# Performance work log

Hardware: AMD Instinct MI355X
Metric: run time of the kernel (lower is better)

Reference implementation:

```python
import jax, jax.numpy as jnp
import numpy as np

B, H, S, D = 2, 16, 2048, 64

def setup_inputs() -> dict:
    key = jax.random.key(0)
    kq, kk, kv, km = jax.random.split(key, 4)
    q = jax.random.normal(kq, (B, H, S, D), dtype=jnp.float32)
    k = jax.random.normal(kk, (B, H, S, D), dtype=jnp.float32)
    v = jax.random.normal(kv, (B, H, S, D), dtype=jnp.float32)
    mask = jax.random.randint(km, (B, 1, S, S), 0, 2, dtype=jnp.int32)
    return {"q": q, "k": k, "v": v, "mask": mask}

def reference(q, k, v, mask):
    d_k = q.shape[-1]
    # scores: [B, H, S, S]
    scores = jnp.einsum('bhqd,bhkd->bhqk', q, k) / jnp.sqrt(jnp.float32(d_k))
    scores = jnp.where(mask == 0, -jnp.inf, scores)
    attn = jax.nn.softmax(scores, axis=-1)
    return jnp.einsum('bhqk,bhkd->bhqd', attn, v)
```

## Files before the change

### kernel.cpp

```cpp
#include <hip/hip_runtime.h>
#include <hip/hip_bf16.h>

typedef unsigned short u16;
typedef unsigned int   u32;
typedef unsigned long long u64;
typedef __attribute__((ext_vector_type(8)))  __bf16 bf16x8;
typedef __attribute__((ext_vector_type(4)))  float  f32x4;
typedef __attribute__((ext_vector_type(16))) float  f32x16;
typedef __attribute__((ext_vector_type(8)))  u16    ushort8;
typedef __attribute__((ext_vector_type(4)))  u32    u32x4;

#define S_LEN 2048
#define D_DIM 64
#define NBH   32
#define SD    131072
#define MROW  32
#define MB_PB 65536
#define NT    32

#define KB_OFF 0u
#define VT_OFF 8388608u
#define MB_OFF 16777216u
#define WS_NEED 17825792u

#define QSCALE 0.18033688011112042f

static __device__ __forceinline__ u16 f2bf(float f) {
  u32 u = __builtin_bit_cast(u32, f);
  u += 0x7fffu + ((u >> 16) & 1u);
  return (u16)(u >> 16);
}

static __device__ __forceinline__ void gl16(const void* g, void* l) {
  __builtin_amdgcn_global_load_lds(
      (const __attribute__((address_space(1))) u32*)g,
      (__attribute__((address_space(3))) u32*)l, 16, 0, 0);
}

static __device__ __forceinline__ u32 cvtpk(float lo, float hi) {
  u32 d;
  asm("v_cvt_pk_bf16_f32 %0, %1, %2" : "=v"(d) : "v"(lo), "v"(hi));
  return d;
}
static __device__ __forceinline__ void plswap(u32& a, u32& b) {
  asm volatile("v_permlane32_swap_b32 %0, %1" : "+v"(a), "+v"(b));
}

#define WAITV(N) asm volatile("s_waitcnt vmcnt(" #N ")" ::: "memory")

__global__ __launch_bounds__(256) void prep_all(
    const float* __restrict__ K, const float* __restrict__ V, const int* __restrict__ M,
    u16* __restrict__ Kb, u16* __restrict__ Vt, u64* __restrict__ Mb) {
  const int bx = blockIdx.x, tid = threadIdx.x;
  if (bx < 2048) {
    size_t i = ((size_t)bx * 256 + tid) * 8;
    float4 a = *reinterpret_cast<const float4*>(K + i);
    float4 b = *reinterpret_cast<const float4*>(K + i + 4);
    ushort8 u;
    u[0]=f2bf(a.x); u[1]=f2bf(a.y); u[2]=f2bf(a.z); u[3]=f2bf(a.w);
    u[4]=f2bf(b.x); u[5]=f2bf(b.y); u[6]=f2bf(b.z); u[7]=f2bf(b.w);
    *reinterpret_cast<ushort8*>(Kb + i) = u;
  } else if (bx < 3072) {
    __shared__ u16 t[64][72];
    const int idx = bx - 2048;
    const int bh = idx >> 5, s0 = (idx & 31) * 64;
    const float* src = V + ((size_t)bh * S_LEN + s0) * D_DIM;
    const int r = tid >> 2, c0 = (tid & 3) * 16;
#pragma unroll
    for (int i = 0; i < 16; i += 4) {
      float4 x = *reinterpret_cast<const float4*>(src + r * 64 + c0 + i);
      t[r][c0+i]   = f2bf(x.x); t[r][c0+i+1] = f2bf(x.y);
      t[r][c0+i+2] = f2bf(x.z); t[r][c0+i+3] = f2bf(x.w);
    }
    __syncthreads();
    u16* dst = Vt + (size_t)bh * SD + s0;
#pragma unroll
    for (int qq = 0; qq < 2; ++qq) {
      int q = tid * 2 + qq;
      int d = q >> 3, so = (q & 7) * 8;
      ushort8 u;
#pragma unroll
      for (int j = 0; j < 8; ++j) u[j] = t[so + j][d];
      *reinterpret_cast<ushort8*>(dst + d * S_LEN + so) = u;
    }
  } else {
    int g = (bx - 3072) * 256 + tid;
    int lane = g & 63;
    int v = M[(size_t)g];
    u64 bits = __ballot(v != 0);
    if (lane == 0) Mb[g >> 6] = bits;
  }
}

static __device__ __forceinline__ void iter_body(
    const u16* kb, const u16* vb, u64 mw,
    const bf16x8* Qf, f32x16& accOT0, f32x16& accOT1, float& l_,
    int l31, int hi, int swz) {
  const u32 mlo = (u32)mw, mhiw = (u32)(mw >> 32);

  f32x16 sT0 = {0,0,0,0,0,0,0,0,0,0,0,0,0,0,0,0};
  f32x16 sT1 = {0,0,0,0,0,0,0,0,0,0,0,0,0,0,0,0};
  __builtin_amdgcn_s_setprio(1);
#pragma unroll
  for (int s = 0; s < 4; ++s) {
    bf16x8 k0 = *reinterpret_cast<const bf16x8*>(kb + l31 * 64        + ((s*2+hi) ^ swz) * 8);
    bf16x8 k1 = *reinterpret_cast<const bf16x8*>(kb + (32 + l31) * 64 + ((s*2+hi) ^ swz) * 8);
    sT0 = __builtin_amdgcn_mfma_f32_32x32x16_bf16(k0, Qf[s], sT0, 0, 0, 0);
    sT1 = __builtin_amdgcn_mfma_f32_32x32x16_bf16(k1, Qf[s], sT1, 0, 0, 0);
  }
  __builtin_amdgcn_s_setprio(0);

  float lp0 = 0.f, lp1 = 0.f, lp2 = 0.f, lp3 = 0.f;
  u32 A0_[8], A1_[8];
#pragma unroll
  for (int T = 0; T < 2; ++T) {
    const f32x16& sv = T ? sT1 : sT0;
    const u32 mword = T ? mhiw : mlo;
    float pr[16];
#pragma unroll
    for (int r = 0; r < 16; ++r) {
      const int bit = (r & 3) + 8 * (r >> 2) + 4 * hi;
      float e = __builtin_amdgcn_exp2f(sv[r]);
      int sx = __builtin_amdgcn_sbfe(mword, bit, 1);
      e = __builtin_bit_cast(float, __builtin_bit_cast(u32, e) & (u32)sx);
      if ((r & 3) == 0) lp0 += e; else if ((r & 3) == 1) lp1 += e;
      else if ((r & 3) == 2) lp2 += e; else lp3 += e;
      pr[r] = e;
    }
#pragma unroll
    for (int j = 0; j < 8; ++j) {
      u32 w = cvtpk(pr[2 * j], pr[2 * j + 1]);
      if (T == 0) A0_[j] = w; else A1_[j] = w;
    }
  }
  l_ += (lp0 + lp1) + (lp2 + lp3);

  bf16x8 PA[4];
  {
    u32 a, c, b2, d2;
    a = A0_[0]; c = A0_[2]; plswap(a, c);
    b2 = A0_[1]; d2 = A0_[3]; plswap(b2, d2);
    u32x4 w0 = {a, b2, c, d2}; PA[0] = __builtin_bit_cast(bf16x8, w0);
    a = A0_[4]; c = A0_[6]; plswap(a, c);
    b2 = A0_[5]; d2 = A0_[7]; plswap(b2, d2);
    u32x4 w1 = {a, b2, c, d2}; PA[1] = __builtin_bit_cast(bf16x8, w1);
    a = A1_[0]; c = A1_[2]; plswap(a, c);
    b2 = A1_[1]; d2 = A1_[3]; plswap(b2, d2);
    u32x4 w2 = {a, b2, c, d2}; PA[2] = __builtin_bit_cast(bf16x8, w2);
    a = A1_[4]; c = A1_[6]; plswap(a, c);
    b2 = A1_[5]; d2 = A1_[7]; plswap(b2, d2);
    u32x4 w3 = {a, b2, c, d2}; PA[3] = __builtin_bit_cast(bf16x8, w3);
  }

  __builtin_amdgcn_s_setprio(1);
#pragma unroll
  for (int ks = 0; ks < 4; ++ks) {
    bf16x8 v0 = *reinterpret_cast<const bf16x8*>(vb + l31 * 64        + ((ks*2+hi) ^ swz) * 8);
    bf16x8 v1 = *reinterpret_cast<const bf16x8*>(vb + (32 + l31) * 64 + ((ks*2+hi) ^ swz) * 8);
    accOT0 = __builtin_amdgcn_mfma_f32_32x32x16_bf16(v0, PA[ks], accOT0, 0, 0, 0);
    accOT1 = __builtin_amdgcn_mfma_f32_32x32x16_bf16(v1, PA[ks], accOT1, 0, 0, 0);
  }
  __builtin_amdgcn_s_setprio(0);
}

__global__ __launch_bounds__(256, 2) void attn_fwd5(
    const float* __restrict__ Q, const u16* __restrict__ Kb,
    const u16* __restrict__ Vt, const u64* __restrict__ Mb,
    float* __restrict__ O) {
  __shared__ __align__(16) u16 LB[32768];

  const int tid  = threadIdx.x;
  const int lane = tid & 63;
  const int wid  = tid >> 6;
  const int l31  = lane & 31;
  const int hi   = lane >> 5;
  const int swz  = l31 & 7;

  const int bh = blockIdx.y, b = bh >> 4;
  const int q0w = blockIdx.x * 128 + wid * 32;
  const size_t base = (size_t)bh * SD;

  bf16x8 Qf[4];
  {
    const float* qsrc = Q + base + (size_t)(q0w + l31) * 64;
#pragma unroll
    for (int s = 0; s < 4; ++s) {
      const int d0 = s * 16 + hi * 8;
      float4 x = *reinterpret_cast<const float4*>(qsrc + d0);
      float4 y = *reinterpret_cast<const float4*>(qsrc + d0 + 4);
      u32x4 w;
      w[0] = cvtpk(x.x * QSCALE, x.y * QSCALE);
      w[1] = cvtpk(x.z * QSCALE, x.w * QSCALE);
      w[2] = cvtpk(y.x * QSCALE, y.y * QSCALE);
      w[3] = cvtpk(y.z * QSCALE, y.w * QSCALE);
      Qf[s] = __builtin_bit_cast(bf16x8, w);
    }
  }

  const int srow = tid >> 3;
  const int sjx  = (tid & 7) ^ (srow & 7);
  const u16* ksA = Kb + base + srow * 64 + sjx * 8;
  const u16* vsA = Vt + base + (size_t)srow * S_LEN + sjx * 8;

  const u64* mp = Mb + (size_t)b * MB_PB + (size_t)(q0w + l31) * MROW;

  f32x16 accOT0 = {0,0,0,0,0,0,0,0,0,0,0,0,0,0,0,0};
  f32x16 accOT1 = {0,0,0,0,0,0,0,0,0,0,0,0,0,0,0,0};
  float l_ = 0.f;

#define STAGE(buf, it) do {                                                        \
    gl16(ksA + (size_t)(it) * 4096,        LB + (buf) * 4096 + tid * 8);           \
    gl16(ksA + (size_t)(it) * 4096 + 2048, LB + (buf) * 4096 + 2048 + tid * 8);    \
    gl16(vsA + (size_t)(it) * 64,          LB + 16384 + (buf) * 4096 + tid * 8);   \
    gl16(vsA + (size_t)(it) * 64 + 65536,  LB + 16384 + (buf) * 4096 + 2048 + tid * 8); \
  } while (0)

#define BODY(IT, J, WN, DOSTAGE) do {                                    \
    WAITV(WN);                                                            \
    __builtin_amdgcn_s_barrier();                                         \
    __builtin_amdgcn_sched_barrier(0);                                    \
    if (DOSTAGE) { STAGE((((J) + 3) & 3), (IT) + 3); }                    \
    iter_body(LB + (J) * 4096, LB + 16384 + (J) * 4096, cm[J],            \
              Qf, accOT0, accOT1, l_, l31, hi, swz);                      \
  } while (0)

  u64 cm[4], nm[4];
  cm[0] = mp[0]; cm[1] = mp[1]; cm[2] = mp[2]; cm[3] = mp[3];
  STAGE(0, 0); STAGE(1, 1); STAGE(2, 2);

#pragma unroll 1
  for (int g = 0; g < 7; ++g) {
    const int it0 = g * 4;
    nm[0] = mp[it0 + 4]; nm[1] = mp[it0 + 5];
    nm[2] = mp[it0 + 6]; nm[3] = mp[it0 + 7];
    BODY(it0 + 0, 0, 8, true);
    BODY(it0 + 1, 1, 8, true);
    BODY(it0 + 2, 2, 8, true);
    BODY(it0 + 3, 3, 8, true);
    cm[0] = nm[0]; cm[1] = nm[1]; cm[2] = nm[2]; cm[3] = nm[3];
  }
  BODY(28, 0, 8, true);
  BODY(29, 1, 8, false);
  BODY(30, 2, 4, false);
  BODY(31, 3, 0, false);

  __syncthreads();

  l_ += __shfl_xor(l_, 32);
  const float inv = __builtin_amdgcn_rcpf(l_);

  float* Sc = (float*)((char*)LB + wid * 4608);
#pragma unroll
  for (int D0 = 0; D0 < 2; ++D0) {
    const f32x16& acc = D0 ? accOT1 : accOT0;
#pragma unroll
    for (int r = 0; r < 16; ++r) {
      const int dloc = (r & 3) + 8 * (r >> 2) + 4 * hi;
      Sc[l31 * 36 + dloc] = acc[r] * inv;
    }
    asm volatile("s_waitcnt lgkmcnt(0)" ::: "memory");
    __builtin_amdgcn_sched_barrier(0);
    const int qq = lane >> 1, off = (lane & 1) * 16;
#pragma unroll
    for (int j = 0; j < 4; ++j) {
      float4 x = *reinterpret_cast<const float4*>(&Sc[qq * 36 + off + j * 4]);
      *reinterpret_cast<float4*>(O + base + (size_t)(q0w + qq) * 64 + D0 * 32 + off + j * 4) = x;
    }
    asm volatile("s_waitcnt lgkmcnt(0)" ::: "memory");
    __builtin_amdgcn_sched_barrier(0);
  }
#undef STAGE
#undef BODY
}

#define KST 72
#define VST 40
#define PST 40
static __device__ __forceinline__ bf16x8 ld_frag(const u16* p) {
  ushort8 u = *reinterpret_cast<const ushort8*>(p);
  return __builtin_bit_cast(bf16x8, u);
}
__global__ __launch_bounds__(256) void attn_fwd_v1(
    const float* __restrict__ Q, const float* __restrict__ K,
    const float* __restrict__ V, const int* __restrict__ M,
    float* __restrict__ O) {
  __shared__ __align__(16) u16 Klds[32 * KST];
  __shared__ __align__(16) u16 Vlds[64 * VST];
  __shared__ __align__(16) u16 Plds[4 * 16 * PST];
  const int tid = threadIdx.x, lane = tid & 63, wid = tid >> 6;
  const int lrow = lane & 15, lgrp = lane >> 4;
  const int bh = blockIdx.y, b = bh >> 4;
  const int q0 = blockIdx.x * 64 + wid * 16;
  const int base = bh * S_LEN * D_DIM, mbase = b * S_LEN * S_LEN;
  bf16x8 qf[2];
#pragma unroll
  for (int c = 0; c < 2; ++c) {
    const float* src = Q + base + (q0 + lrow) * 64 + c * 32 + lgrp * 8;
    float4 x = *reinterpret_cast<const float4*>(src);
    float4 y = *reinterpret_cast<const float4*>(src + 4);
    ushort8 u;
    u[0]=f2bf(x.x*0.125f); u[1]=f2bf(x.y*0.125f); u[2]=f2bf(x.z*0.125f); u[3]=f2bf(x.w*0.125f);
    u[4]=f2bf(y.x*0.125f); u[5]=f2bf(y.y*0.125f); u[6]=f2bf(y.z*0.125f); u[7]=f2bf(y.w*0.125f);
    qf[c] = __builtin_bit_cast(bf16x8, u);
  }
  f32x4 accO[4];
#pragma unroll
  for (int c = 0; c < 4; ++c) accO[c] = (f32x4){0.f,0.f,0.f,0.f};
  float m_[4] = {-1e9f,-1e9f,-1e9f,-1e9f}, l_[4] = {0.f,0.f,0.f,0.f};
  const int srow = tid >> 3, scol = (tid & 7) * 8;
  for (int kv0 = 0; kv0 < S_LEN; kv0 += 32) {
    __syncthreads();
    {
      const float* src = K + base + (kv0 + srow) * 64 + scol;
      float4 x = *reinterpret_cast<const float4*>(src);
      float4 y = *reinterpret_cast<const float4*>(src + 4);
      ushort8 u;
      u[0]=f2bf(x.x); u[1]=f2bf(x.y); u[2]=f2bf(x.z); u[3]=f2bf(x.w);
      u[4]=f2bf(y.x); u[5]=f2bf(y.y); u[6]=f2bf(y.z); u[7]=f2bf(y.w);
      *reinterpret_cast<ushort8*>(&Klds[srow * KST + scol]) = u;
    }
    {
      const float* src = V + base + (kv0 + srow) * 64 + scol;
      float4 x = *reinterpret_cast<const float4*>(src);
      float4 y = *reinterpret_cast<const float4*>(src + 4);
      float vals[8] = {x.x,x.y,x.z,x.w,y.x,y.y,y.z,y.w};
#pragma unroll
      for (int i = 0; i < 8; ++i) Vlds[(scol + i) * VST + srow] = f2bf(vals[i]);
    }
    __syncthreads();
    f32x4 s0 = (f32x4){0.f,0.f,0.f,0.f}, s1 = (f32x4){0.f,0.f,0.f,0.f};
#pragma unroll
    for (int c = 0; c < 2; ++c) {
      bf16x8 k0 = ld_frag(&Klds[lrow * KST + c * 32 + lgrp * 8]);
      bf16x8 k1 = ld_frag(&Klds[(16 + lrow) * KST + c * 32 + lgrp * 8]);
      s0 = __builtin_amdgcn_mfma_f32_16x16x32_bf16(qf[c], k0, s0, 0, 0, 0);
      s1 = __builtin_amdgcn_mfma_f32_16x16x32_bf16(qf[c], k1, s1, 0, 0, 0);
    }
#pragma unroll
    for (int r = 0; r < 4; ++r) {
      const int moff = mbase + (q0 + lgrp * 4 + r) * S_LEN + kv0 + lrow;
      if (M[moff] == 0)      s0[r] = -1e30f;
      if (M[moff + 16] == 0) s1[r] = -1e30f;
    }
    const int pbase = wid * 16 * PST;
#pragma unroll
    for (int r = 0; r < 4; ++r) {
      float t = fmaxf(s0[r], s1[r]);
      t = fmaxf(t, __shfl_xor(t, 1)); t = fmaxf(t, __shfl_xor(t, 2));
      t = fmaxf(t, __shfl_xor(t, 4)); t = fmaxf(t, __shfl_xor(t, 8));
      float mn = fmaxf(m_[r], t);
      float sf = __expf(m_[r] - mn);
      m_[r] = mn;
      float p0 = __expf(s0[r] - mn), p1 = __expf(s1[r] - mn);
      float su = p0 + p1;
      su += __shfl_xor(su, 1); su += __shfl_xor(su, 2);
      su += __shfl_xor(su, 4); su += __shfl_xor(su, 8);
      l_[r] = l_[r] * sf + su;
      accO[0][r] *= sf; accO[1][r] *= sf; accO[2][r] *= sf; accO[3][r] *= sf;
      const int prow = lgrp * 4 + r;
      Plds[pbase + prow * PST + lrow]      = f2bf(p0);
      Plds[pbase + prow * PST + 16 + lrow] = f2bf(p1);
    }
    asm volatile("s_waitcnt lgkmcnt(0)" ::: "memory");
    __builtin_amdgcn_sched_barrier(0);
    bf16x8 pa = ld_frag(&Plds[pbase + lrow * PST + lgrp * 8]);
#pragma unroll
    for (int c = 0; c < 4; ++c) {
      bf16x8 bv = ld_frag(&Vlds[(c * 16 + lrow) * VST + lgrp * 8]);
      accO[c] = __builtin_amdgcn_mfma_f32_16x16x32_bf16(pa, bv, accO[c], 0, 0, 0);
    }
  }
#pragma unroll
  for (int r = 0; r < 4; ++r) {
    const float inv = 1.0f / l_[r];
    float* dst = O + base + (q0 + lgrp * 4 + r) * 64;
#pragma unroll
    for (int c = 0; c < 4; ++c) dst[c * 16 + lrow] = accO[c][r] * inv;
  }
}

extern "C" void kernel_launch(void* const* d_in, const int* in_sizes, int n_in,
                              void* d_out, int out_size, void* d_ws, size_t ws_size,
                              hipStream_t stream) {
  const float* q = (const float*)d_in[0];
  const float* k = (const float*)d_in[1];
  const float* v = (const float*)d_in[2];
  const int*   m = (const int*)d_in[3];
  float* out = (float*)d_out;

  if (ws_size < (size_t)WS_NEED) {
    dim3 grid(S_LEN / 64, NBH);
    attn_fwd_v1<<<grid, dim3(256), 0, stream>>>(q, k, v, m, out);
    return;
  }

  u16* Kb = (u16*)((char*)d_ws + KB_OFF);
  u16* Vt = (u16*)((char*)d_ws + VT_OFF);
  u64* Mb = (u64*)((char*)d_ws + MB_OFF);

  prep_all<<<dim3(35840), dim3(256), 0, stream>>>(k, v, m, Kb, Vt, Mb);
  attn_fwd5<<<dim3(S_LEN / 128, NBH), dim3(256), 0, stream>>>(q, Kb, Vt, Mb, out);
}
```

Before: 75.10 us.

## Load K/V fragments directly from global into registers, dropping LDS staging

Replaces the LDS-staged, 4-deep async pipeline for K and V with direct global-to-register loads: K fragments are double-buffered in registers across iterations and V fragments are loaded before the softmax. The V transpose is padded (row stride 2080) to avoid cache-set conflicts on strided reads, and the exp/mask loop is interleaved with packing. This removes LDS traffic and the wait/barrier machinery, but each wave now fetches K/V independently through L1/L2 with less latency hiding, and a per-iteration barrier is kept.

```diff
diff --git a/kernel.cpp b/kernel.cpp
--- a/kernel.cpp
+++ b/kernel.cpp
@@ -18,10 +18,13 @@
 #define MB_PB 65536
 #define NT    32
 
+#define VTS   2080
+#define VT_BH 133120
+
 #define KB_OFF 0u
 #define VT_OFF 8388608u
-#define MB_OFF 16777216u
-#define WS_NEED 17825792u
+#define MB_OFF 16908288u
+#define WS_NEED 18087936u
 
 #define QSCALE 0.18033688011112042f
 
@@ -31,12 +34,6 @@
   return (u16)(u >> 16);
 }
 
-static __device__ __forceinline__ void gl16(const void* g, void* l) {
-  __builtin_amdgcn_global_load_lds(
-      (const __attribute__((address_space(1))) u32*)g,
-      (__attribute__((address_space(3))) u32*)l, 16, 0, 0);
-}
-
 static __device__ __forceinline__ u32 cvtpk(float lo, float hi) {
   u32 d;
   asm("v_cvt_pk_bf16_f32 %0, %1, %2" : "=v"(d) : "v"(lo), "v"(hi));
@@ -45,8 +42,6 @@
 static __device__ __forceinline__ void plswap(u32& a, u32& b) {
   asm volatile("v_permlane32_swap_b32 %0, %1" : "+v"(a), "+v"(b));
 }
-
-#define WAITV(N) asm volatile("s_waitcnt vmcnt(" #N ")" ::: "memory")
 
 __global__ __launch_bounds__(256) void prep_all(
     const float* __restrict__ K, const float* __restrict__ V, const int* __restrict__ M,
@@ -73,7 +68,7 @@
       t[r][c0+i+2] = f2bf(x.z); t[r][c0+i+3] = f2bf(x.w);
     }
     __syncthreads();
-    u16* dst = Vt + (size_t)bh * SD + s0;
+    u16* dst = Vt + (size_t)bh * VT_BH + s0;
 #pragma unroll
     for (int qq = 0; qq < 2; ++qq) {
       int q = tid * 2 + qq;
@@ -81,7 +76,7 @@
       ushort8 u;
 #pragma unroll
       for (int j = 0; j < 8; ++j) u[j] = t[so + j][d];
-      *reinterpret_cast<ushort8*>(dst + d * S_LEN + so) = u;
+      *reinterpret_cast<ushort8*>(dst + (size_t)d * VTS + so) = u;
     }
   } else {
     int g = (bx - 3072) * 256 + tid;
@@ -92,10 +87,18 @@
   }
 }
 
+
+static __device__ __forceinline__ void loadK(bf16x8 (&Kf)[8], const u16* kp) {
+#pragma unroll
+  for (int s = 0; s < 4; ++s) {
+    Kf[s]     = *reinterpret_cast<const bf16x8*>(kp + s * 16 - 1024);
+    Kf[s + 4] = *reinterpret_cast<const bf16x8*>(kp + s * 16 + 1024);
+  }
+}
+
 static __device__ __forceinline__ void iter_body(
-    const u16* kb, const u16* vb, u64 mw,
-    const bf16x8* Qf, f32x16& accOT0, f32x16& accOT1, float& l_,
-    int l31, int hi, int swz) {
+    const bf16x8 (&Kf)[8], const u16* vp0, const u16* vp1, u64 mw,
+    const bf16x8 (&Qf)[4], f32x16& accOT0, f32x16& accOT1, float& l_, int hi) {
   const u32 mlo = (u32)mw, mhiw = (u32)(mw >> 32);
 
   f32x16 sT0 = {0,0,0,0,0,0,0,0,0,0,0,0,0,0,0,0};
@@ -103,37 +106,42 @@
   __builtin_amdgcn_s_setprio(1);
 #pragma unroll
   for (int s = 0; s < 4; ++s) {
-    bf16x8 k0 = *reinterpret_cast<const bf16x8*>(kb + l31 * 64        + ((s*2+hi) ^ swz) * 8);
-    bf16x8 k1 = *reinterpret_cast<const bf16x8*>(kb + (32 + l31) * 64 + ((s*2+hi) ^ swz) * 8);
-    sT0 = __builtin_amdgcn_mfma_f32_32x32x16_bf16(k0, Qf[s], sT0, 0, 0, 0);
-    sT1 = __builtin_amdgcn_mfma_f32_32x32x16_bf16(k1, Qf[s], sT1, 0, 0, 0);
+    sT0 = __builtin_amdgcn_mfma_f32_32x32x16_bf16(Kf[s],     Qf[s], sT0, 0, 0, 0);
+    sT1 = __builtin_amdgcn_mfma_f32_32x32x16_bf16(Kf[s + 4], Qf[s], sT1, 0, 0, 0);
   }
   __builtin_amdgcn_s_setprio(0);
 
-  float lp0 = 0.f, lp1 = 0.f, lp2 = 0.f, lp3 = 0.f;
+  bf16x8 Vf[8];
+#pragma unroll
+  for (int ks = 0; ks < 4; ++ks) {
+    Vf[ks]     = *reinterpret_cast<const bf16x8*>(vp0 + ks * 16);
+    Vf[ks + 4] = *reinterpret_cast<const bf16x8*>(vp1 + ks * 16);
+  }
+  __builtin_amdgcn_sched_barrier(0);
+
+  float lp0 = 0.f, lp1 = 0.f;
   u32 A0_[8], A1_[8];
 #pragma unroll
   for (int T = 0; T < 2; ++T) {
     const f32x16& sv = T ? sT1 : sT0;
     const u32 mword = T ? mhiw : mlo;
-    float pr[16];
-#pragma unroll
-    for (int r = 0; r < 16; ++r) {
-      const int bit = (r & 3) + 8 * (r >> 2) + 4 * hi;
-      float e = __builtin_amdgcn_exp2f(sv[r]);
-      int sx = __builtin_amdgcn_sbfe(mword, bit, 1);
-      e = __builtin_bit_cast(float, __builtin_bit_cast(u32, e) & (u32)sx);
-      if ((r & 3) == 0) lp0 += e; else if ((r & 3) == 1) lp1 += e;
-      else if ((r & 3) == 2) lp2 += e; else lp3 += e;
-      pr[r] = e;
-    }
 #pragma unroll
     for (int j = 0; j < 8; ++j) {
-      u32 w = cvtpk(pr[2 * j], pr[2 * j + 1]);
+      const int r0 = 2 * j, r1 = 2 * j + 1;
+      const int b0 = (r0 & 3) + 8 * (r0 >> 2) + 4 * hi;
+      const int b1 = (r1 & 3) + 8 * (r1 >> 2) + 4 * hi;
+      float e0 = __builtin_amdgcn_exp2f(sv[r0]);
+      float e1 = __builtin_amdgcn_exp2f(sv[r1]);
+      int s0 = __builtin_amdgcn_sbfe(mword, b0, 1);
+      int s1 = __builtin_amdgcn_sbfe(mword, b1, 1);
+      e0 = __builtin_bit_cast(float, __builtin_bit_cast(u32, e0) & (u32)s0);
+      e1 = __builtin_bit_cast(float, __builtin_bit_cast(u32, e1) & (u32)s1);
+      lp0 += e0; lp1 += e1;
+      u32 w = cvtpk(e0, e1);
       if (T == 0) A0_[j] = w; else A1_[j] = w;
     }
   }
-  l_ += (lp0 + lp1) + (lp2 + lp3);
+  l_ += lp0 + lp1;
 
   bf16x8 PA[4];
   {
@@ -155,26 +163,25 @@
   __builtin_amdgcn_s_setprio(1);
 #pragma unroll
   for (int ks = 0; ks < 4; ++ks) {
-    bf16x8 v0 = *reinterpret_cast<const bf16x8*>(vb + l31 * 64        + ((ks*2+hi) ^ swz) * 8);
-    bf16x8 v1 = *reinterpret_cast<const bf16x8*>(vb + (32 + l31) * 64 + ((ks*2+hi) ^ swz) * 8);
-    accOT0 = __builtin_amdgcn_mfma_f32_32x32x16_bf16(v0, PA[ks], accOT0, 0, 0, 0);
-    accOT1 = __builtin_amdgcn_mfma_f32_32x32x16_bf16(v1, PA[ks], accOT1, 0, 0, 0);
+    accOT0 = __builtin_amdgcn_mfma_f32_32x32x16_bf16(Vf[ks],     PA[ks], accOT0, 0, 0, 0);
+    accOT1 = __builtin_amdgcn_mfma_f32_32x32x16_bf16(Vf[ks + 4], PA[ks], accOT1, 0, 0, 0);
   }
   __builtin_amdgcn_s_setprio(0);
-}
-
-__global__ __launch_bounds__(256, 2) void attn_fwd5(
+
+  __builtin_amdgcn_s_barrier();
+}
+
+__global__ __launch_bounds__(256, 2) void attn_fwd7(
     const float* __restrict__ Q, const u16* __restrict__ Kb,
     const u16* __restrict__ Vt, const u64* __restrict__ Mb,
     float* __restrict__ O) {
-  __shared__ __align__(16) u16 LB[32768];
+  __shared__ __align__(16) float Sc[4 * 1152];
 
   const int tid  = threadIdx.x;
   const int lane = tid & 63;
   const int wid  = tid >> 6;
   const int l31  = lane & 31;
   const int hi   = lane >> 5;
-  const int swz  = l31 & 7;
 
   const int bh = blockIdx.y, b = bh >> 4;
   const int q0w = blockIdx.x * 128 + wid * 32;
@@ -197,10 +204,10 @@
     }
   }
 
-  const int srow = tid >> 3;
-  const int sjx  = (tid & 7) ^ (srow & 7);
-  const u16* ksA = Kb + base + srow * 64 + sjx * 8;
-  const u16* vsA = Vt + base + (size_t)srow * S_LEN + sjx * 8;
+  const u16* kpE = Kb + base + l31 * 64 + hi * 8 + 1024;
+  const u16* kpO = kpE + 4096;
+  const u16* vp0 = Vt + (size_t)bh * VT_BH + (size_t)l31 * VTS + hi * 8;
+  const u16* vp1 = vp0 + 32 * VTS;
 
   const u64* mp = Mb + (size_t)b * MB_PB + (size_t)(q0w + l31) * MROW;
 
@@ -208,69 +215,48 @@
   f32x16 accOT1 = {0,0,0,0,0,0,0,0,0,0,0,0,0,0,0,0};
   float l_ = 0.f;
 
-#define STAGE(buf, it) do {                                                        \
-    gl16(ksA + (size_t)(it) * 4096,        LB + (buf) * 4096 + tid * 8);           \
-    gl16(ksA + (size_t)(it) * 4096 + 2048, LB + (buf) * 4096 + 2048 + tid * 8);    \
-    gl16(vsA + (size_t)(it) * 64,          LB + 16384 + (buf) * 4096 + tid * 8);   \
-    gl16(vsA + (size_t)(it) * 64 + 65536,  LB + 16384 + (buf) * 4096 + 2048 + tid * 8); \
-  } while (0)
-
-#define BODY(IT, J, WN, DOSTAGE) do {                                    \
-    WAITV(WN);                                                            \
-    __builtin_amdgcn_s_barrier();                                         \
-    __builtin_amdgcn_sched_barrier(0);                                    \
-    if (DOSTAGE) { STAGE((((J) + 3) & 3), (IT) + 3); }                    \
-    iter_body(LB + (J) * 4096, LB + 16384 + (J) * 4096, cm[J],            \
-              Qf, accOT0, accOT1, l_, l31, hi, swz);                      \
-  } while (0)
-
-  u64 cm[4], nm[4];
-  cm[0] = mp[0]; cm[1] = mp[1]; cm[2] = mp[2]; cm[3] = mp[3];
-  STAGE(0, 0); STAGE(1, 1); STAGE(2, 2);
+  bf16x8 KfA[8], KfB[8];
+  loadK(KfA, kpE);
+  u64 mwC0 = mp[0], mwC1 = mp[1];
 
 #pragma unroll 1
-  for (int g = 0; g < 7; ++g) {
-    const int it0 = g * 4;
-    nm[0] = mp[it0 + 4]; nm[1] = mp[it0 + 5];
-    nm[2] = mp[it0 + 6]; nm[3] = mp[it0 + 7];
-    BODY(it0 + 0, 0, 8, true);
-    BODY(it0 + 1, 1, 8, true);
-    BODY(it0 + 2, 2, 8, true);
-    BODY(it0 + 3, 3, 8, true);
-    cm[0] = nm[0]; cm[1] = nm[1]; cm[2] = nm[2]; cm[3] = nm[3];
-  }
-  BODY(28, 0, 8, true);
-  BODY(29, 1, 8, false);
-  BODY(30, 2, 4, false);
-  BODY(31, 3, 0, false);
-
-  __syncthreads();
+  for (int t = 0; t < 16; ++t) {
+    u64 mwN0 = mp[2 * t + 2], mwN1 = mp[2 * t + 3];
+
+    loadK(KfB, kpO);
+    iter_body(KfA, vp0, vp1, mwC0, Qf, accOT0, accOT1, l_, hi);
+
+    kpE += 8192; kpO += 8192;
+    loadK(KfA, kpE);
+    iter_body(KfB, vp0 + 64, vp1 + 64, mwC1, Qf, accOT0, accOT1, l_, hi);
+
+    vp0 += 128; vp1 += 128;
+    mwC0 = mwN0; mwC1 = mwN1;
+  }
 
   l_ += __shfl_xor(l_, 32);
   const float inv = __builtin_amdgcn_rcpf(l_);
 
-  float* Sc = (float*)((char*)LB + wid * 4608);
+  float* sc = Sc + wid * 1152;
 #pragma unroll
   for (int D0 = 0; D0 < 2; ++D0) {
     const f32x16& acc = D0 ? accOT1 : accOT0;
 #pragma unroll
     for (int r = 0; r < 16; ++r) {
       const int dloc = (r & 3) + 8 * (r >> 2) + 4 * hi;
-      Sc[l31 * 36 + dloc] = acc[r] * inv;
+      sc[l31 * 36 + dloc] = acc[r] * inv;
     }
     asm volatile("s_waitcnt lgkmcnt(0)" ::: "memory");
     __builtin_amdgcn_sched_barrier(0);
     const int qq = lane >> 1, off = (lane & 1) * 16;
 #pragma unroll
     for (int j = 0; j < 4; ++j) {
-      float4 x = *reinterpret_cast<const float4*>(&Sc[qq * 36 + off + j * 4]);
+      float4 x = *reinterpret_cast<const float4*>(&sc[qq * 36 + off + j * 4]);
       *reinterpret_cast<float4*>(O + base + (size_t)(q0w + qq) * 64 + D0 * 32 + off + j * 4) = x;
     }
     asm volatile("s_waitcnt lgkmcnt(0)" ::: "memory");
     __builtin_amdgcn_sched_barrier(0);
   }
-#undef STAGE
-#undef BODY
 }
 
 #define KST 72
@@ -399,5 +385,5 @@
   u64* Mb = (u64*)((char*)d_ws + MB_OFF);
 
   prep_all<<<dim3(35840), dim3(256), 0, stream>>>(k, v, m, Kb, Vt, Mb);
-  attn_fwd5<<<dim3(S_LEN / 128, NBH), dim3(256), 0, stream>>>(q, Kb, Vt, Mb, out);
-}
+  attn_fwd7<<<dim3(S_LEN / 128, NBH), dim3(256), 0, stream>>>(q, Kb, Vt, Mb, out);
+}
```

Result: slower. 126.6 us (+68.5%).

## Pre-pack K and V into MFMA fragment order for contiguous LDS reads

Applied to the files above, without the earlier changes.

The prep kernel now writes K and V as bf16 tiles already arranged in the per-lane MFMA operand order. The attention kernel can then stage them with fully contiguous global-to-LDS copies and read each operand as lane*8, with no XOR swizzle address math. This removes the strided transposed V store and the index arithmetic in the inner loop. The softmax exp/mask loop is also restructured to work in pairs and uses two partial sums instead of four, which shortens the dependency chains less. The cost is a more complex prep pass, where both K and V now go through an LDS shuffle.

```diff
diff --git a/kernel.cpp b/kernel.cpp
--- a/kernel.cpp
+++ b/kernel.cpp
@@ -18,10 +18,12 @@
 #define MB_PB 65536
 #define NT    32
 
-#define KB_OFF 0u
-#define VT_OFF 8388608u
+#define FR_BH 131072
+
+#define KF_OFF 0u
+#define VF_OFF 8388608u
 #define MB_OFF 16777216u
-#define WS_NEED 17825792u
+#define WS_NEED 17833984u
 
 #define QSCALE 0.18033688011112042f
 
@@ -50,21 +52,14 @@
 
 __global__ __launch_bounds__(256) void prep_all(
     const float* __restrict__ K, const float* __restrict__ V, const int* __restrict__ M,
-    u16* __restrict__ Kb, u16* __restrict__ Vt, u64* __restrict__ Mb) {
+    u16* __restrict__ Kf, u16* __restrict__ Vf, u64* __restrict__ Mb) {
   const int bx = blockIdx.x, tid = threadIdx.x;
   if (bx < 2048) {
-    size_t i = ((size_t)bx * 256 + tid) * 8;
-    float4 a = *reinterpret_cast<const float4*>(K + i);
-    float4 b = *reinterpret_cast<const float4*>(K + i + 4);
-    ushort8 u;
-    u[0]=f2bf(a.x); u[1]=f2bf(a.y); u[2]=f2bf(a.z); u[3]=f2bf(a.w);
-    u[4]=f2bf(b.x); u[5]=f2bf(b.y); u[6]=f2bf(b.z); u[7]=f2bf(b.w);
-    *reinterpret_cast<ushort8*>(Kb + i) = u;
-  } else if (bx < 3072) {
     __shared__ u16 t[64][72];
-    const int idx = bx - 2048;
-    const int bh = idx >> 5, s0 = (idx & 31) * 64;
-    const float* src = V + ((size_t)bh * S_LEN + s0) * D_DIM;
+    const bool isK = bx < 1024;
+    const int idx = isK ? bx : bx - 1024;
+    const int bh = idx >> 5, tt = idx & 31;
+    const float* src = (isK ? K : V) + ((size_t)bh * S_LEN + tt * 64) * D_DIM;
     const int r = tid >> 2, c0 = (tid & 3) * 16;
 #pragma unroll
     for (int i = 0; i < 16; i += 4) {
@@ -73,18 +68,23 @@
       t[r][c0+i+2] = f2bf(x.z); t[r][c0+i+3] = f2bf(x.w);
     }
     __syncthreads();
-    u16* dst = Vt + (size_t)bh * SD + s0;
+    u16* dst = (isK ? Kf : Vf) + (size_t)bh * FR_BH + (size_t)tt * 4096;
 #pragma unroll
     for (int qq = 0; qq < 2; ++qq) {
-      int q = tid * 2 + qq;
-      int d = q >> 3, so = (q & 7) * 8;
+      const int f = tid * 2 + qq;
+      const int sp = f >> 7, half = (f >> 6) & 1, l = f & 63;
       ushort8 u;
-#pragma unroll
-      for (int j = 0; j < 8; ++j) u[j] = t[so + j][d];
-      *reinterpret_cast<ushort8*>(dst + d * S_LEN + so) = u;
+      if (isK) {
+        u = *reinterpret_cast<const ushort8*>(&t[half * 32 + (l & 31)][sp * 16 + (l >> 5) * 8]);
+      } else {
+        const int kv0 = sp * 16 + (l >> 5) * 8, d = half * 32 + (l & 31);
+#pragma unroll
+        for (int j = 0; j < 8; ++j) u[j] = t[kv0 + j][d];
+      }
+      *reinterpret_cast<ushort8*>(dst + (size_t)f * 8) = u;
     }
   } else {
-    int g = (bx - 3072) * 256 + tid;
+    int g = (bx - 2048) * 256 + tid;
     int lane = g & 63;
     int v = M[(size_t)g];
     u64 bits = __ballot(v != 0);
@@ -95,7 +95,7 @@
 static __device__ __forceinline__ void iter_body(
     const u16* kb, const u16* vb, u64 mw,
     const bf16x8* Qf, f32x16& accOT0, f32x16& accOT1, float& l_,
-    int l31, int hi, int swz) {
+    int lane, int hi) {
   const u32 mlo = (u32)mw, mhiw = (u32)(mw >> 32);
 
   f32x16 sT0 = {0,0,0,0,0,0,0,0,0,0,0,0,0,0,0,0};
@@ -103,37 +103,36 @@
   __builtin_amdgcn_s_setprio(1);
 #pragma unroll
   for (int s = 0; s < 4; ++s) {
-    bf16x8 k0 = *reinterpret_cast<const bf16x8*>(kb + l31 * 64        + ((s*2+hi) ^ swz) * 8);
-    bf16x8 k1 = *reinterpret_cast<const bf16x8*>(kb + (32 + l31) * 64 + ((s*2+hi) ^ swz) * 8);
+    bf16x8 k0 = *reinterpret_cast<const bf16x8*>(kb + s * 1024 + lane * 8);
+    bf16x8 k1 = *reinterpret_cast<const bf16x8*>(kb + s * 1024 + 512 + lane * 8);
     sT0 = __builtin_amdgcn_mfma_f32_32x32x16_bf16(k0, Qf[s], sT0, 0, 0, 0);
     sT1 = __builtin_amdgcn_mfma_f32_32x32x16_bf16(k1, Qf[s], sT1, 0, 0, 0);
   }
   __builtin_amdgcn_s_setprio(0);
 
-  float lp0 = 0.f, lp1 = 0.f, lp2 = 0.f, lp3 = 0.f;
+  float lp0 = 0.f, lp1 = 0.f;
   u32 A0_[8], A1_[8];
 #pragma unroll
   for (int T = 0; T < 2; ++T) {
     const f32x16& sv = T ? sT1 : sT0;
     const u32 mword = T ? mhiw : mlo;
-    float pr[16];
-#pragma unroll
-    for (int r = 0; r < 16; ++r) {
-      const int bit = (r & 3) + 8 * (r >> 2) + 4 * hi;
-      float e = __builtin_amdgcn_exp2f(sv[r]);
-      int sx = __builtin_amdgcn_sbfe(mword, bit, 1);
-      e = __builtin_bit_cast(float, __builtin_bit_cast(u32, e) & (u32)sx);
-      if ((r & 3) == 0) lp0 += e; else if ((r & 3) == 1) lp1 += e;
-      else if ((r & 3) == 2) lp2 += e; else lp3 += e;
-      pr[r] = e;
-    }
 #pragma unroll
     for (int j = 0; j < 8; ++j) {
-      u32 w = cvtpk(pr[2 * j], pr[2 * j + 1]);
+      const int r0 = 2 * j, r1 = 2 * j + 1;
+      const int b0 = (r0 & 3) + 8 * (r0 >> 2) + 4 * hi;
+      const int b1 = (r1 & 3) + 8 * (r1 >> 2) + 4 * hi;
+      float e0 = __builtin_amdgcn_exp2f(sv[r0]);
+      float e1 = __builtin_amdgcn_exp2f(sv[r1]);
+      int s0 = __builtin_amdgcn_sbfe(mword, b0, 1);
+      int s1 = __builtin_amdgcn_sbfe(mword, b1, 1);
+      e0 = __builtin_bit_cast(float, __builtin_bit_cast(u32, e0) & (u32)s0);
+      e1 = __builtin_bit_cast(float, __builtin_bit_cast(u32, e1) & (u32)s1);
+      lp0 += e0; lp1 += e1;
+      u32 w = cvtpk(e0, e1);
       if (T == 0) A0_[j] = w; else A1_[j] = w;
     }
   }
-  l_ += (lp0 + lp1) + (lp2 + lp3);
+  l_ += lp0 + lp1;
 
   bf16x8 PA[4];
   {
@@ -155,17 +154,17 @@
   __builtin_amdgcn_s_setprio(1);
 #pragma unroll
   for (int ks = 0; ks < 4; ++ks) {
-    bf16x8 v0 = *reinterpret_cast<const bf16x8*>(vb + l31 * 64        + ((ks*2+hi) ^ swz) * 8);
-    bf16x8 v1 = *reinterpret_cast<const bf16x8*>(vb + (32 + l31) * 64 + ((ks*2+hi) ^ swz) * 8);
+    bf16x8 v0 = *reinterpret_cast<const bf16x8*>(vb + ks * 1024 + lane * 8);
+    bf16x8 v1 = *reinterpret_cast<const bf16x8*>(vb + ks * 1024 + 512 + lane * 8);
     accOT0 = __builtin_amdgcn_mfma_f32_32x32x16_bf16(v0, PA[ks], accOT0, 0, 0, 0);
     accOT1 = __builtin_amdgcn_mfma_f32_32x32x16_bf16(v1, PA[ks], accOT1, 0, 0, 0);
   }
   __builtin_amdgcn_s_setprio(0);
 }
 
-__global__ __launch_bounds__(256, 2) void attn_fwd5(
-    const float* __restrict__ Q, const u16* __restrict__ Kb,
-    const u16* __restrict__ Vt, const u64* __restrict__ Mb,
+__global__ __launch_bounds__(256, 2) void attn_fwd9(
+    const float* __restrict__ Q, const u16* __restrict__ Kf,
+    const u16* __restrict__ Vf, const u64* __restrict__ Mb,
     float* __restrict__ O) {
   __shared__ __align__(16) u16 LB[32768];
 
@@ -174,7 +173,6 @@
   const int wid  = tid >> 6;
   const int l31  = lane & 31;
   const int hi   = lane >> 5;
-  const int swz  = l31 & 7;
 
   const int bh = blockIdx.y, b = bh >> 4;
   const int q0w = blockIdx.x * 128 + wid * 32;
@@ -197,10 +195,8 @@
     }
   }
 
-  const int srow = tid >> 3;
-  const int sjx  = (tid & 7) ^ (srow & 7);
-  const u16* ksA = Kb + base + srow * 64 + sjx * 8;
-  const u16* vsA = Vt + base + (size_t)srow * S_LEN + sjx * 8;
+  const u16* kfA = Kf + (size_t)bh * FR_BH;
+  const u16* vfA = Vf + (size_t)bh * FR_BH;
 
   const u64* mp = Mb + (size_t)b * MB_PB + (size_t)(q0w + l31) * MROW;
 
@@ -208,11 +204,11 @@
   f32x16 accOT1 = {0,0,0,0,0,0,0,0,0,0,0,0,0,0,0,0};
   float l_ = 0.f;
 
-#define STAGE(buf, it) do {                                                        \
-    gl16(ksA + (size_t)(it) * 4096,        LB + (buf) * 4096 + tid * 8);           \
-    gl16(ksA + (size_t)(it) * 4096 + 2048, LB + (buf) * 4096 + 2048 + tid * 8);    \
-    gl16(vsA + (size_t)(it) * 64,          LB + 16384 + (buf) * 4096 + tid * 8);   \
-    gl16(vsA + (size_t)(it) * 64 + 65536,  LB + 16384 + (buf) * 4096 + 2048 + tid * 8); \
+#define STAGE(buf, it) do {                                                                  \
+    gl16(kfA + (size_t)(it) * 4096 + tid * 8,        LB + (buf) * 4096 + tid * 8);           \
+    gl16(kfA + (size_t)(it) * 4096 + 2048 + tid * 8, LB + (buf) * 4096 + 2048 + tid * 8);    \
+    gl16(vfA + (size_t)(it) * 4096 + tid * 8,        LB + 16384 + (buf) * 4096 + tid * 8);   \
+    gl16(vfA + (size_t)(it) * 4096 + 2048 + tid * 8, LB + 16384 + (buf) * 4096 + 2048 + tid * 8); \
   } while (0)
 
 #define BODY(IT, J, WN, DOSTAGE) do {                                    \
@@ -221,7 +217,7 @@
     __builtin_amdgcn_sched_barrier(0);                                    \
     if (DOSTAGE) { STAGE((((J) + 3) & 3), (IT) + 3); }                    \
     iter_body(LB + (J) * 4096, LB + 16384 + (J) * 4096, cm[J],            \
-              Qf, accOT0, accOT1, l_, l31, hi, swz);                      \
+              Qf, accOT0, accOT1, l_, lane, hi);                          \
   } while (0)
 
   u64 cm[4], nm[4];
@@ -394,10 +390,10 @@
     return;
   }
 
-  u16* Kb = (u16*)((char*)d_ws + KB_OFF);
-  u16* Vt = (u16*)((char*)d_ws + VT_OFF);
+  u16* Kf = (u16*)((char*)d_ws + KF_OFF);
+  u16* Vf = (u16*)((char*)d_ws + VF_OFF);
   u64* Mb = (u64*)((char*)d_ws + MB_OFF);
 
-  prep_all<<<dim3(35840), dim3(256), 0, stream>>>(k, v, m, Kb, Vt, Mb);
-  attn_fwd5<<<dim3(S_LEN / 128, NBH), dim3(256), 0, stream>>>(q, Kb, Vt, Mb, out);
-}
+  prep_all<<<dim3(34816), dim3(256), 0, stream>>>(k, v, m, Kf, Vf, Mb);
+  attn_fwd9<<<dim3(S_LEN / 128, NBH), dim3(256), 0, stream>>>(q, Kf, Vf, Mb, out);
+}
```

New measurement: 77.23 us. +2.8%, slower.
